# Performance work log

Measured on AMD Instinct MI355X. Metric: run time of the kernel, lower is better.

## Reference

```python
import jax, jax.numpy as jnp
import numpy as np

N, D = 2, 256
M, L, K, DV = 8, 4, 4, 32
LK = L * K
LEVEL_HW = [(96, 96), (48, 48), (24, 24), (12, 12)]
S = sum(h * w for h, w in LEVEL_HW)  # 12240 flattened pyramid tokens
Q = S
OFFSET_SCALE = 0.5  # sampling_offset_scale_factor


def setup_inputs() -> dict:
    ks = jax.random.split(jax.random.key(0), 16)
    def lin(k, din, dout):
        return jax.random.normal(k, (din, dout), jnp.float32) / np.sqrt(din)
    return {
        "queries": jax.random.normal(ks[0], (N, Q, D), jnp.float32),
        "query_geometries": jax.random.uniform(ks[1], (N, Q, 4), jnp.float32, minval=0.1, maxval=0.9),
        "src_values": jax.random.normal(ks[2], (N, S, D), jnp.float32),
        "W_off": lin(ks[3], D, M * LK * 2) * 0.01,
        "b_off": jax.random.normal(ks[4], (M * LK * 2,), jnp.float32),
        "W_attn": lin(ks[5], D, M * LK),
        "b_attn": jnp.zeros((M * LK,), jnp.float32),
        "W_val": lin(ks[6], D, M * DV),
        "b_val": jnp.zeros((M * DV,), jnp.float32),
        "W_out": lin(ks[7], M * DV, D),
        "b_out": jnp.zeros((D,), jnp.float32),
    }


def _bilinear_sample(vmap_l, grid):
    # vmap_l: [B, dv, H, W]; grid: [B, Q, K, 2] in [-1, 1]
    # Matches F.grid_sample(mode='bilinear', align_corners=False, padding_mode='zeros')
    B, dv, H, W = vmap_l.shape
    x = (grid[..., 0] + 1.0) * (W / 2) - 0.5
    y = (grid[..., 1] + 1.0) * (H / 2) - 0.5
    x0 = jnp.floor(x)
    y0 = jnp.floor(y)
    wx = x - x0
    wy = y - y0
    x0i = x0.astype(jnp.int32)
    y0i = y0.astype(jnp.int32)
    vflat = vmap_l.reshape(B, dv, H * W)

    def corner(xi, yi, w):
        valid = (xi >= 0) & (xi < W) & (yi >= 0) & (yi < H)
        idx = jnp.clip(yi, 0, H - 1) * W + jnp.clip(xi, 0, W - 1)
        g = jax.vmap(lambda vf, i: vf[:, i])(vflat, idx)  # [B, dv, Q, K]
        return g * (w * valid)[:, None, :, :]

    return (corner(x0i, y0i, (1 - wx) * (1 - wy))
            + corner(x0i + 1, y0i, wx * (1 - wy))
            + corner(x0i, y0i + 1, (1 - wx) * wy)
            + corner(x0i + 1, y0i + 1, wx * wy))


def msdeform(queries, query_geometries, src_values, W_off, b_off, W_attn, b_attn,
             W_val, b_val, W_out, b_out):
    # attention weights: softmax over the L*K samples of each head
    attn = jax.nn.softmax((queries @ W_attn + b_attn).reshape(N, Q, M, LK), axis=-1)
    # predicted sampling offsets [N, Q, M, LK, 2]
    off = (queries @ W_off + b_off).reshape(N, Q, M, LK, 2)
    xy = query_geometries[..., :2]
    wh = query_geometries[..., 2:]
    scale = wh * (OFFSET_SCALE / K)  # wh * kv_count_per_level_inverse * sampling_offset_max_value
    pos = xy[:, :, None, None, :] + off * scale[:, :, None, None, :]  # normalized [0,1]
    # collapse (batch, head) -> B = N*M, rescale to [-1,1] for grid_sample semantics
    grid = (2.0 * pos - 1.0).transpose(0, 2, 1, 3, 4).reshape(N * M, Q, LK, 2)
    # project values and rebuild the per-level feature maps
    v = (src_values @ W_val + b_val).reshape(N, S, M, DV)
    samples, s = [], 0
    for l, (H, W) in enumerate(LEVEL_HW):
        vl = v[:, s:s + H * W].reshape(N, H, W, M, DV).transpose(0, 3, 4, 1, 2).reshape(N * M, DV, H, W)
        samples.append(_bilinear_sample(vl, grid[:, :, l * K:(l + 1) * K]))  # [N*M, DV, Q, K]
        s += H * W
    sampled = jnp.concatenate(samples, axis=-1)  # [N*M, DV, Q, LK]
    aw = attn.transpose(0, 2, 1, 3).reshape(N * M, 1, Q, LK)
    out = (sampled * aw).sum(-1)  # weighted reduction -> [N*M, DV, Q]
    out = out.reshape(N, M, DV, Q).transpose(0, 3, 1, 2).reshape(N, Q, M * DV)
    return out @ W_out + b_out  # backprojector


def reference(queries, query_geometries, src_values, W_off, b_off, W_attn, b_attn,
              W_val, b_val, W_out, b_out):
    return msdeform(queries, query_geometries, src_values, W_off, b_off, W_attn,
                    b_attn, W_val, b_val, W_out, b_out)
```

## Files before the change

kernel.cpp:

```cpp
#include <hip/hip_runtime.h>
#include <hip/hip_bf16.h>
#include <hip/hip_fp16.h>
#include <cstddef>

#define NB 2
#define QN 12240
#define SN 12240
#define MREAL 24480
#define MPAD  24576
#define MT    192

typedef unsigned short ushortT;
typedef unsigned int uintT;
typedef __bf16 bf16x8 __attribute__((ext_vector_type(8)));
typedef float f32x4 __attribute__((ext_vector_type(4)));

__device__ __forceinline__ ushortT f2bf(float f) {
    uintT u = __float_as_uint(f);
    uintT r = u + 0x7fffu + ((u >> 16) & 1u);
    return (ushortT)(r >> 16);
}
__device__ __forceinline__ float bf_lo(uintT u) {
    return __uint_as_float(u << 16);
}
__device__ __forceinline__ float bf_hi(uintT u) {
    return __uint_as_float(u & 0xffff0000u);
}

__device__ __forceinline__ void async_ld16(const ushortT* g, ushortT* l) {
    __builtin_amdgcn_global_load_lds(
        (const __attribute__((address_space(1))) unsigned int*)g,
        (__attribute__((address_space(3))) unsigned int*)l, 16, 0, 0);
}

__global__ __launch_bounds__(256) void cast_all(
    const float* __restrict__ q, const float* __restrict__ src,
    const float* __restrict__ Wval, const float* __restrict__ Wattn,
    const float* __restrict__ Woff, const float* __restrict__ Wout,
    ushortT* __restrict__ qb, ushortT* __restrict__ sb,
    ushortT* __restrict__ tval, ushortT* __restrict__ tlo,
    ushortT* __restrict__ tout)
{
    int bx = blockIdx.x;
    if (bx < 6120) {
        const int issrc = bx >= 3060;
        const size_t idx = ((size_t)(bx - (issrc ? 3060 : 0)) * 256 + threadIdx.x) * 8;
        const float* in = issrc ? src : q;
        ushortT* out = issrc ? sb : qb;
        const float4 a = *(const float4*)(in + idx);
        const float4 b = *(const float4*)(in + idx + 4);
        uint4 o;
        o.x = (uintT)f2bf(a.x) | ((uintT)f2bf(a.y) << 16);
        o.y = (uintT)f2bf(a.z) | ((uintT)f2bf(a.w) << 16);
        o.z = (uintT)f2bf(b.x) | ((uintT)f2bf(b.y) << 16);
        o.w = (uintT)f2bf(b.z) | ((uintT)f2bf(b.w) << 16);
        *(uint4*)(out + idx) = o;
        return;
    }
    bx -= 6120;
    const float* W; ushortT* T; int n, Nw, trow;
    if (bx < 256)      { W = Wval;  T = tval; n = bx;       Nw = 256; trow = n; }
    else if (bx < 384) { W = Wattn; T = tlo;  n = bx - 256; Nw = 128; trow = n; }
    else if (bx < 640) { W = Woff;  T = tlo;  n = bx - 384; Nw = 256; trow = n + 128; }
    else               { W = Wout;  T = tout; n = bx - 640; Nw = 256; trow = n; }
    const int k = threadIdx.x;
    T[(size_t)trow * 256 + k] = f2bf(W[(size_t)k * Nw + n]);
}

__global__ __launch_bounds__(256) void gemm_vlo(
    const ushortT* __restrict__ q_bf, const ushortT* __restrict__ src_bf,
    const ushortT* __restrict__ wt_val, const ushortT* __restrict__ wt_lo,
    const float* __restrict__ b_val, const float* __restrict__ b_attn,
    const float* __restrict__ b_off,
    ushortT* __restrict__ v_bf, float* __restrict__ lo_ws)
{
    const int z = blockIdx.x >= 2;
    const int col0 = (z ? blockIdx.x - 2 : blockIdx.x) * 128;

    __shared__ __attribute__((aligned(16))) ushortT As[128 * 32];
    __shared__ __attribute__((aligned(16))) ushortT Bs[128 * 32];

    const ushortT* A  = z ? q_bf : src_bf;
    const ushortT* Bt = z ? wt_lo : wt_val;

    const int tid  = threadIdx.x;
    const int wave = tid >> 6;
    const int lane = tid & 63;
    const int row0 = blockIdx.y * 128;
    const int wr = (wave >> 1) * 64;
    const int wc = (wave & 1) * 64;

    f32x4 acc[4][4];
    #pragma unroll
    for (int i = 0; i < 4; i++)
        #pragma unroll
        for (int j = 0; j < 4; j++)
            acc[i][j] = (f32x4)0.f;

    const int srow = (lane >> 2);
    const int sk8  = (lane & 3) * 8;

    for (int k0 = 0; k0 < 256; k0 += 32) {
        #pragma unroll
        for (int j = 0; j < 2; j++) {
            const int r = wave * 32 + j * 16;
            async_ld16(A  + (size_t)(row0 + r + srow) * 256 + k0 + sk8, &As[r * 32]);
            async_ld16(Bt + (size_t)(col0 + r + srow) * 256 + k0 + sk8, &Bs[r * 32]);
        }
        __syncthreads();

        bf16x8 af[4], bfr[4];
        const int mrow = lane & 15;
        const int kq   = (lane >> 4) * 8;
        #pragma unroll
        for (int i = 0; i < 4; i++) {
            af[i]  = *(const bf16x8*)&As[(wr + i * 16 + mrow) * 32 + kq];
            bfr[i] = *(const bf16x8*)&Bs[(wc + i * 16 + mrow) * 32 + kq];
        }
        #pragma unroll
        for (int i = 0; i < 4; i++)
            #pragma unroll
            for (int j = 0; j < 4; j++)
                acc[i][j] = __builtin_amdgcn_mfma_f32_16x16x32_bf16(
                    af[i], bfr[j], acc[i][j], 0, 0, 0);
        __syncthreads();
    }

    const float* bp = z ? ((col0 < 128) ? b_attn : b_off) : b_val;
    const int cofs  = (z && col0 >= 128) ? 128 : 0;

    #pragma unroll
    for (int i = 0; i < 4; i++) {
        const int rbase = row0 + wr + i * 16 + ((lane >> 4) << 2);
        #pragma unroll
        for (int j = 0; j < 4; j++) {
            const int col = col0 + wc + j * 16 + (lane & 15);
            const float bb = bp[col - cofs];
            #pragma unroll
            for (int r = 0; r < 4; r++) {
                const int row = rbase + r;
                if (row < MREAL) {
                    const float val = acc[i][j][r] + bb;
                    if (z) lo_ws[(size_t)row * 384 + col] = val;
                    else   v_bf[(size_t)row * 256 + col] = f2bf(val);
                }
            }
        }
    }
}

__global__ __launch_bounds__(256) void gemm_out(
    const ushortT* __restrict__ A, const ushortT* __restrict__ Bt,
    const float* __restrict__ bias, float* __restrict__ C)
{
    __shared__ __attribute__((aligned(16))) ushortT As[128 * 32];
    __shared__ __attribute__((aligned(16))) ushortT Bs[128 * 32];

    const int tid  = threadIdx.x;
    const int wave = tid >> 6;
    const int lane = tid & 63;
    const int row0 = blockIdx.y * 128;
    const int col0 = blockIdx.x * 128;
    const int wr = (wave >> 1) * 64;
    const int wc = (wave & 1) * 64;

    f32x4 acc[4][4];
    #pragma unroll
    for (int i = 0; i < 4; i++)
        #pragma unroll
        for (int j = 0; j < 4; j++)
            acc[i][j] = (f32x4)0.f;

    const int srow = (lane >> 2);
    const int sk8  = (lane & 3) * 8;

    for (int k0 = 0; k0 < 256; k0 += 32) {
        #pragma unroll
        for (int j = 0; j < 2; j++) {
            const int r = wave * 32 + j * 16;
            async_ld16(A  + (size_t)(row0 + r + srow) * 256 + k0 + sk8, &As[r * 32]);
            async_ld16(Bt + (size_t)(col0 + r + srow) * 256 + k0 + sk8, &Bs[r * 32]);
        }
        __syncthreads();

        bf16x8 af[4], bfr[4];
        const int mrow = lane & 15;
        const int kq   = (lane >> 4) * 8;
        #pragma unroll
        for (int i = 0; i < 4; i++) {
            af[i]  = *(const bf16x8*)&As[(wr + i * 16 + mrow) * 32 + kq];
            bfr[i] = *(const bf16x8*)&Bs[(wc + i * 16 + mrow) * 32 + kq];
        }
        #pragma unroll
        for (int i = 0; i < 4; i++)
            #pragma unroll
            for (int j = 0; j < 4; j++)
                acc[i][j] = __builtin_amdgcn_mfma_f32_16x16x32_bf16(
                    af[i], bfr[j], acc[i][j], 0, 0, 0);
        __syncthreads();
    }

    #pragma unroll
    for (int i = 0; i < 4; i++) {
        const int rbase = row0 + wr + i * 16 + ((lane >> 4) << 2);
        #pragma unroll
        for (int j = 0; j < 4; j++) {
            const int col = col0 + wc + j * 16 + (lane & 15);
            const float bb = bias[col];
            #pragma unroll
            for (int r = 0; r < 4; r++) {
                const int row = rbase + r;
                if (row < MREAL)
                    C[(size_t)row * 256 + col] = acc[i][j][r] + bb;
            }
        }
    }
}

__global__ __launch_bounds__(256) void sample_kernel(
    const float* __restrict__ lo,
    const float* __restrict__ geom,
    const ushortT* __restrict__ v,
    ushortT* __restrict__ out)
{
    const int tid  = threadIdx.x;
    const int w    = tid >> 6;
    const int lane = tid & 63;
    const int m    = lane >> 3;
    const int n    = blockIdx.y;
    const int q0   = blockIdx.x << 2;

    __shared__ __attribute__((aligned(16))) int pls[4][544];

    const size_t qb = (size_t)n * QN + q0 + w;

    {
        const int p = lane & 7;
        const float* lorow = lo + qb * 384;
        const float2 lg = *(const float2*)(lorow + m * 16 + p * 2);
        const float4 of = *(const float4*)(lorow + 128 + m * 32 + p * 4);
        const float4 g  = *(const float4*)(geom + qb * 4);

        float mx = fmaxf(lg.x, lg.y);
        mx = fmaxf(mx, __shfl_xor(mx, 1));
        mx = fmaxf(mx, __shfl_xor(mx, 2));
        mx = fmaxf(mx, __shfl_xor(mx, 4));
        const float e0 = __expf(lg.x - mx);
        const float e1 = __expf(lg.y - mx);
        float s = e0 + e1;
        s += __shfl_xor(s, 1);
        s += __shfl_xor(s, 2);
        s += __shfl_xor(s, 4);
        const float inv = 1.f / s;

        const int l  = p >> 1;
        const int Wl = 96 >> l;
        const int s0 = (l == 0) ? 0 : (l == 1) ? 9216 : (l == 2) ? 11520 : 12096;
        const float cx = g.x, cy = g.y;
        const float sx = g.z * 0.125f, sy = g.w * 0.125f;
        int* myrec = &pls[w][m * 68 + p * 8];

        #pragma unroll
        for (int t = 0; t < 2; t++) {
            const float ox = t ? of.z : of.x;
            const float oy = t ? of.w : of.y;
            const float wa = (t ? e1 : e0) * inv;

            const float x = (cx + ox * sx) * (float)Wl - 0.5f;
            const float y = (cy + oy * sy) * (float)Wl - 0.5f;
            const float xf = floorf(x), yf = floorf(y);
            const int x0 = (int)xf, y0 = (int)yf;
            const float wx = x - xf, wy = y - yf;

            const bool vx0 = (x0 >= 0) & (x0 < Wl);
            const bool vx1 = (x0 + 1 >= 0) & (x0 + 1 < Wl);
            const bool vy0 = (y0 >= 0) & (y0 < Wl);
            const bool vy1 = (y0 + 1 >= 0) & (y0 + 1 < Wl);

            const float w00 = (vx0 & vy0) ? wa * (1.f - wx) * (1.f - wy) : 0.f;
            const float w10 = (vx1 & vy0) ? wa * wx * (1.f - wy) : 0.f;
            const float w01 = (vx0 & vy1) ? wa * (1.f - wx) * wy : 0.f;
            const float w11 = (vx1 & vy1) ? wa * wx * wy : 0.f;

            const int xc0 = min(max(x0, 0), Wl - 1);
            const int xc1 = min(max(x0 + 1, 0), Wl - 1);
            const int yc0 = min(max(y0, 0), Wl - 1);
            const int yc1 = min(max(y0 + 1, 0), Wl - 1);

            const int iv0   = (s0 + yc0 * Wl + xc0) << 9;
            const int dx    = (xc1 - xc0) << 9;
            const int dyrow = ((yc1 - yc0) * Wl) << 9;
            __half2 h01 = __floats2half2_rn(w00, w10);
            __half2 h23 = __floats2half2_rn(w01, w11);
            int4 rec;
            rec.x = iv0;
            rec.y = dx | (dyrow << 16);
            rec.z = *reinterpret_cast<int*>(&h01);
            rec.w = *reinterpret_cast<int*>(&h23);
            *(int4*)(myrec + t * 4) = rec;
        }
    }
    __syncthreads();

    const int c = lane & 7;
    const int chan_byte = (m * 32 + c * 4) * 2;
    const unsigned char* vb =
        (const unsigned char*)(v + (size_t)n * SN * 256);
    const int* grec = &pls[w][m * 68];

    float a0 = 0.f, a1 = 0.f, a2 = 0.f, a3 = 0.f;

    #pragma unroll
    for (int lk = 0; lk < 16; lk++) {
        const int4 rec = *(const int4*)(grec + lk * 4);
        const int base = rec.x + chan_byte;
        const int dx   = rec.y & 0xffff;
        const int dy   = ((uintT)rec.y) >> 16;

        const uint2 u0 = *(const uint2*)(vb + base);
        const uint2 u1 = *(const uint2*)(vb + base + dx);
        const uint2 u2 = *(const uint2*)(vb + base + dy);
        const uint2 u3 = *(const uint2*)(vb + base + dy + dx);

        const __half2 h01 = *reinterpret_cast<const __half2*>(&rec.z);
        const __half2 h23 = *reinterpret_cast<const __half2*>(&rec.w);
        const float2 wlo = __half22float2(h01);
        const float2 whi = __half22float2(h23);

        a0 += wlo.x * bf_lo(u0.x) + wlo.y * bf_lo(u1.x) + whi.x * bf_lo(u2.x) + whi.y * bf_lo(u3.x);
        a1 += wlo.x * bf_hi(u0.x) + wlo.y * bf_hi(u1.x) + whi.x * bf_hi(u2.x) + whi.y * bf_hi(u3.x);
        a2 += wlo.x * bf_lo(u0.y) + wlo.y * bf_lo(u1.y) + whi.x * bf_lo(u2.y) + whi.y * bf_lo(u3.y);
        a3 += wlo.x * bf_hi(u0.y) + wlo.y * bf_hi(u1.y) + whi.x * bf_hi(u2.y) + whi.y * bf_hi(u3.y);
    }

    ushort4 o;
    o.x = f2bf(a0); o.y = f2bf(a1); o.z = f2bf(a2); o.w = f2bf(a3);
    *(ushort4*)(out + qb * 256 + m * 32 + c * 4) = o;
}

extern "C" void kernel_launch(void* const* d_in, const int* in_sizes, int n_in,
                              void* d_out, int out_size, void* d_ws, size_t ws_size,
                              hipStream_t stream)
{
    const float* queries = (const float*)d_in[0];
    const float* geom    = (const float*)d_in[1];
    const float* src     = (const float*)d_in[2];
    const float* W_off   = (const float*)d_in[3];
    const float* b_off   = (const float*)d_in[4];
    const float* W_attn  = (const float*)d_in[5];
    const float* b_attn  = (const float*)d_in[6];
    const float* W_val   = (const float*)d_in[7];
    const float* b_val   = (const float*)d_in[8];
    const float* W_out   = (const float*)d_in[9];
    const float* b_out   = (const float*)d_in[10];
    float* out = (float*)d_out;

    ushortT* wsb = (ushortT*)d_ws;
    const size_t PADROW = (size_t)MPAD * 256;
    ushortT* q_bf    = wsb;
    ushortT* srcmdv  = wsb + PADROW;
    ushortT* v_bf    = wsb + 2 * PADROW;
    ushortT* wt_val  = wsb + 3 * PADROW;
    ushortT* wt_lo   = wt_val + 65536;
    ushortT* wt_out  = wt_lo + 98304;
    float* lo_ws = (float*)(wt_out + 65536);

    dim3 blk(256);

    cast_all<<<dim3(7016), blk, 0, stream>>>(
        queries, src, W_val, W_attn, W_off, W_out,
        q_bf, srcmdv, wt_val, wt_lo, wt_out);

    gemm_vlo<<<dim3(5, MT), blk, 0, stream>>>(
        q_bf, srcmdv, wt_val, wt_lo, b_val, b_attn, b_off, v_bf, lo_ws);

    sample_kernel<<<dim3(QN / 4, NB), blk, 0, stream>>>(
        lo_ws, geom, v_bf, srcmdv);

    gemm_out<<<dim3(2, MT), blk, 0, stream>>>(srcmdv, wt_out, b_out, out);
}
```

Before: 208.0 us.

## Load GEMM fragments directly from global memory instead of staging through LDS

Removes the LDS staging buffers and the global_load_lds async copies in both GEMM kernels. Each wave now reads its bf16x8 MFMA fragments straight from global memory through a shared helper, with the k-loop unrolled by two and no barriers. This drops the per-step __syncthreads and LDS traffic. In exchange, operands are no longer shared across waves in a block, so each A/B tile is read from global memory (or L2) twice, and the per-lane 16-byte strided accesses may coalesce poorly.

```diff
diff --git a/kernel.cpp b/kernel.cpp
--- a/kernel.cpp
+++ b/kernel.cpp
@@ -25,12 +25,6 @@
 }
 __device__ __forceinline__ float bf_hi(uintT u) {
     return __uint_as_float(u & 0xffff0000u);
-}
-
-__device__ __forceinline__ void async_ld16(const ushortT* g, ushortT* l) {
-    __builtin_amdgcn_global_load_lds(
-        (const __attribute__((address_space(1))) unsigned int*)g,
-        (__attribute__((address_space(3))) unsigned int*)l, 16, 0, 0);
 }
 
 __global__ __launch_bounds__(256) void cast_all(
@@ -67,6 +61,34 @@
     T[(size_t)trow * 256 + k] = f2bf(W[(size_t)k * Nw + n]);
 }
 
+__device__ __forceinline__ void gemm_core_128(
+    const ushortT* __restrict__ A, const ushortT* __restrict__ Bt,
+    int row0, int col0, int lane, int wr, int wc, f32x4 acc[4][4])
+{
+    const int mrow = lane & 15;
+    const int kq   = (lane >> 4) * 8;
+
+    const ushortT* Ap = A  + (size_t)(row0 + wr + mrow) * 256 + kq;
+    const ushortT* Bp = Bt + (size_t)(col0 + wc + mrow) * 256 + kq;
+
+    #pragma unroll 2
+    for (int k0 = 0; k0 < 256; k0 += 32) {
+        bf16x8 af[4], bfr[4];
+        #pragma unroll
+        for (int i = 0; i < 4; i++)
+            af[i] = *(const bf16x8*)(Ap + (size_t)i * 16 * 256 + k0);
+        #pragma unroll
+        for (int j = 0; j < 4; j++)
+            bfr[j] = *(const bf16x8*)(Bp + (size_t)j * 16 * 256 + k0);
+        #pragma unroll
+        for (int i = 0; i < 4; i++)
+            #pragma unroll
+            for (int j = 0; j < 4; j++)
+                acc[i][j] = __builtin_amdgcn_mfma_f32_16x16x32_bf16(
+                    af[i], bfr[j], acc[i][j], 0, 0, 0);
+    }
+}
+
 __global__ __launch_bounds__(256) void gemm_vlo(
     const ushortT* __restrict__ q_bf, const ushortT* __restrict__ src_bf,
     const ushortT* __restrict__ wt_val, const ushortT* __restrict__ wt_lo,
@@ -76,10 +98,6 @@
 {
     const int z = blockIdx.x >= 2;
     const int col0 = (z ? blockIdx.x - 2 : blockIdx.x) * 128;
-
-    __shared__ __attribute__((aligned(16))) ushortT As[128 * 32];
-    __shared__ __attribute__((aligned(16))) ushortT Bs[128 * 32];
-
     const ushortT* A  = z ? q_bf : src_bf;
     const ushortT* Bt = z ? wt_lo : wt_val;
 
@@ -97,34 +115,7 @@
         for (int j = 0; j < 4; j++)
             acc[i][j] = (f32x4)0.f;
 
-    const int srow = (lane >> 2);
-    const int sk8  = (lane & 3) * 8;
-
-    for (int k0 = 0; k0 < 256; k0 += 32) {
-        #pragma unroll
-        for (int j = 0; j < 2; j++) {
-            const int r = wave * 32 + j * 16;
-            async_ld16(A  + (size_t)(row0 + r + srow) * 256 + k0 + sk8, &As[r * 32]);
-            async_ld16(Bt + (size_t)(col0 + r + srow) * 256 + k0 + sk8, &Bs[r * 32]);
-        }
-        __syncthreads();
-
-        bf16x8 af[4], bfr[4];
-        const int mrow = lane & 15;
-        const int kq   = (lane >> 4) * 8;
-        #pragma unroll
-        for (int i = 0; i < 4; i++) {
-            af[i]  = *(const bf16x8*)&As[(wr + i * 16 + mrow) * 32 + kq];
-            bfr[i] = *(const bf16x8*)&Bs[(wc + i * 16 + mrow) * 32 + kq];
-        }
-        #pragma unroll
-        for (int i = 0; i < 4; i++)
-            #pragma unroll
-            for (int j = 0; j < 4; j++)
-                acc[i][j] = __builtin_amdgcn_mfma_f32_16x16x32_bf16(
-                    af[i], bfr[j], acc[i][j], 0, 0, 0);
-        __syncthreads();
-    }
+    gemm_core_128(A, Bt, row0, col0, lane, wr, wc, acc);
 
     const float* bp = z ? ((col0 < 128) ? b_attn : b_off) : b_val;
     const int cofs  = (z && col0 >= 128) ? 128 : 0;
@@ -153,9 +144,6 @@
     const ushortT* __restrict__ A, const ushortT* __restrict__ Bt,
     const float* __restrict__ bias, float* __restrict__ C)
 {
-    __shared__ __attribute__((aligned(16))) ushortT As[128 * 32];
-    __shared__ __attribute__((aligned(16))) ushortT Bs[128 * 32];
-
     const int tid  = threadIdx.x;
     const int wave = tid >> 6;
     const int lane = tid & 63;
@@ -171,34 +159,7 @@
         for (int j = 0; j < 4; j++)
             acc[i][j] = (f32x4)0.f;
 
-    const int srow = (lane >> 2);
-    const int sk8  = (lane & 3) * 8;
-
-    for (int k0 = 0; k0 < 256; k0 += 32) {
-        #pragma unroll
-        for (int j = 0; j < 2; j++) {
-            const int r = wave * 32 + j * 16;
-            async_ld16(A  + (size_t)(row0 + r + srow) * 256 + k0 + sk8, &As[r * 32]);
-            async_ld16(Bt + (size_t)(col0 + r + srow) * 256 + k0 + sk8, &Bs[r * 32]);
-        }
-        __syncthreads();
-
-        bf16x8 af[4], bfr[4];
-        const int mrow = lane & 15;
-        const int kq   = (lane >> 4) * 8;
-        #pragma unroll
-        for (int i = 0; i < 4; i++) {
-            af[i]  = *(const bf16x8*)&As[(wr + i * 16 + mrow) * 32 + kq];
-            bfr[i] = *(const bf16x8*)&Bs[(wc + i * 16 + mrow) * 32 + kq];
-        }
-        #pragma unroll
-        for (int i = 0; i < 4; i++)
-            #pragma unroll
-            for (int j = 0; j < 4; j++)
-                acc[i][j] = __builtin_amdgcn_mfma_f32_16x16x32_bf16(
-                    af[i], bfr[j], acc[i][j], 0, 0, 0);
-        __syncthreads();
-    }
+    gemm_core_128(A, Bt, row0, col0, lane, wr, wc, acc);
 
     #pragma unroll
     for (int i = 0; i < 4; i++) {
```

After: 239.0 us. 14.9% more time.

## Store values head-major and remap sampling threads to queries within one head

Applied to the files above, without the earlier changes.

The value projection now writes its bf16 output as [batch, head, token, channel], so each head's 32 channels form contiguous 64-byte rows. The sampling kernel switches to a grid over (query block, head, batch) with 128-thread blocks. Each wave handles 8 queries of a single head, so gathers read from a compact per-head table that should make better use of cache. The cost is strided, less coalesced stores in the GEMM epilogue, and the per-query offset and logit rows are now read by 8 separate blocks.

```diff
diff --git a/kernel.cpp b/kernel.cpp
--- a/kernel.cpp
+++ b/kernel.cpp
@@ -141,8 +141,14 @@
                 const int row = rbase + r;
                 if (row < MREAL) {
                     const float val = acc[i][j][r] + bb;
-                    if (z) lo_ws[(size_t)row * 384 + col] = val;
-                    else   v_bf[(size_t)row * 256 + col] = f2bf(val);
+                    if (z) {
+                        lo_ws[(size_t)row * 384 + col] = val;
+                    } else {
+                        const int nn = row / SN;
+                        const int s  = row - nn * SN;
+                        const int head = col >> 5, ch = col & 31;
+                        v_bf[(((size_t)nn * 8 + head) * SN + s) * 32 + ch] = f2bf(val);
+                    }
                 }
             }
         }
@@ -217,7 +223,7 @@
     }
 }
 
-__global__ __launch_bounds__(256) void sample_kernel(
+__global__ __launch_bounds__(128) void sample_kernel(
     const float* __restrict__ lo,
     const float* __restrict__ geom,
     const ushortT* __restrict__ v,
@@ -226,13 +232,14 @@
     const int tid  = threadIdx.x;
     const int w    = tid >> 6;
     const int lane = tid & 63;
-    const int m    = lane >> 3;
-    const int n    = blockIdx.y;
-    const int q0   = blockIdx.x << 2;
-
-    __shared__ __attribute__((aligned(16))) int pls[4][544];
-
-    const size_t qb = (size_t)n * QN + q0 + w;
+    const int qi   = lane >> 3;
+    const int m    = blockIdx.y;
+    const int n    = blockIdx.z;
+    const int q    = blockIdx.x * 16 + w * 8 + qi;
+
+    __shared__ __attribute__((aligned(16))) int pls[2][544];
+
+    const size_t qb = (size_t)n * QN + q;
 
     {
         const int p = lane & 7;
@@ -258,7 +265,7 @@
         const int s0 = (l == 0) ? 0 : (l == 1) ? 9216 : (l == 2) ? 11520 : 12096;
         const float cx = g.x, cy = g.y;
         const float sx = g.z * 0.125f, sy = g.w * 0.125f;
-        int* myrec = &pls[w][m * 68 + p * 8];
+        int* myrec = &pls[w][qi * 68 + p * 8];
 
         #pragma unroll
         for (int t = 0; t < 2; t++) {
@@ -287,9 +294,9 @@
             const int yc0 = min(max(y0, 0), Wl - 1);
             const int yc1 = min(max(y0 + 1, 0), Wl - 1);
 
-            const int iv0   = (s0 + yc0 * Wl + xc0) << 9;
-            const int dx    = (xc1 - xc0) << 9;
-            const int dyrow = ((yc1 - yc0) * Wl) << 9;
+            const int iv0   = (s0 + yc0 * Wl + xc0) << 6;
+            const int dx    = (xc1 - xc0) << 6;
+            const int dyrow = ((yc1 - yc0) * Wl) << 6;
             __half2 h01 = __floats2half2_rn(w00, w10);
             __half2 h23 = __floats2half2_rn(w01, w11);
             int4 rec;
@@ -303,17 +310,16 @@
     __syncthreads();
 
     const int c = lane & 7;
-    const int chan_byte = (m * 32 + c * 4) * 2;
-    const unsigned char* vb =
-        (const unsigned char*)(v + (size_t)n * SN * 256);
-    const int* grec = &pls[w][m * 68];
+    const unsigned char* vb = (const unsigned char*)
+        (v + ((size_t)(n * 8 + m) * SN) * 32) + c * 8;
+    const int* grec = &pls[w][qi * 68];
 
     float a0 = 0.f, a1 = 0.f, a2 = 0.f, a3 = 0.f;
 
     #pragma unroll
     for (int lk = 0; lk < 16; lk++) {
         const int4 rec = *(const int4*)(grec + lk * 4);
-        const int base = rec.x + chan_byte;
+        const int base = rec.x;
         const int dx   = rec.y & 0xffff;
         const int dy   = ((uintT)rec.y) >> 16;
 
@@ -374,7 +380,7 @@
     gemm_vlo<<<dim3(5, MT), blk, 0, stream>>>(
         q_bf, srcmdv, wt_val, wt_lo, b_val, b_attn, b_off, v_bf, lo_ws);
 
-    sample_kernel<<<dim3(QN / 4, NB), blk, 0, stream>>>(
+    sample_kernel<<<dim3(QN / 16, 8, NB), dim3(128), 0, stream>>>(
         lo_ws, geom, v_bf, srcmdv);
 
     gemm_out<<<dim3(2, MT), blk, 0, stream>>>(srcmdv, wt_out, b_out, out);
```

Result: no change. 206.5 us (-0.7%).
